# Kernel tuning notes

Measured on AMD Instinct MI355X. Metric: run time of the kernel, lower is better.

Reference implementation:

```python
import jax, jax.numpy as jnp
import numpy as np

L_MAX = 3


def setup_inputs() -> dict:
    key = jax.random.key(0)
    ks = jax.random.split(key, L_MAX + 1)
    n_species, n_samples, n_feat = 2, 1000, 128
    inp = {}
    for l in range(L_MAX + 1):
        inp[f"c_l{l}"] = jax.random.normal(
            ks[l], (n_species, n_samples, 2 * l + 1, n_feat), dtype=jnp.float32
        )
    return inp


def reference(c_l0, c_l1, c_l2, c_l3):
    # For each l: ps = (2l+1)^{-1/2} * sum_m c[..., m, i] * c[..., m, j]
    # i.e. a batched Gram matrix c^T @ c over the m (component) axis,
    # flattened to (S, N, n^2) and concatenated over l.
    parts = []
    for l, c in enumerate((c_l0, c_l1, c_l2, c_l3)):
        cg = (2 * l + 1) ** (-0.5)
        s, n, _, f = c.shape
        ps = cg * jnp.einsum("snmi,snmj->snij", c, c)  # (S, N, f, f)
        parts.append(ps.reshape(s, n, f * f))
    return jnp.concatenate(parts, axis=-1)  # (S, N, (l_max+1)*f^2)
```

## Files before the change

kernel.cpp:

```cpp
#include <hip/hip_runtime.h>


#define NFEAT 128

__device__ __constant__ float kCg[4] = {
    1.0f,
    0.57735026918962576451f,
    0.44721359549995793928f,
    0.37796447300922722721f};

template <int L>
__global__ __launch_bounds__(256) void ps_kernel(const float* __restrict__ c,
                                                 float* __restrict__ out) {
  constexpr int NM = 2 * L + 1;
  __shared__ float sc[NM * NFEAT];

  const int sn  = blockIdx.x;
  const int tid = threadIdx.x;

  const float* src = c + (size_t)sn * (NM * NFEAT);
  if (tid < NM * 32) {
    ((float4*)sc)[tid] = ((const float4*)src)[tid];
  }
  __syncthreads();

  const int j4 = tid & 31;
  const int i0 = tid >> 5;

  float4 b[NM];
#pragma unroll
  for (int m = 0; m < NM; ++m) b[m] = ((const float4*)sc)[m * 32 + j4];

  const float cg = kCg[L];
  float* obase = out + (size_t)sn * (4 * NFEAT * NFEAT) + (size_t)L * (NFEAT * NFEAT);

#pragma unroll
  for (int k = 0; k < 16; ++k) {
    const int i = i0 + 8 * k;
    float4 acc = {0.f, 0.f, 0.f, 0.f};
#pragma unroll
    for (int m = 0; m < NM; ++m) {
      const float a = sc[m * NFEAT + i];
      acc.x += a * b[m].x;
      acc.y += a * b[m].y;
      acc.z += a * b[m].z;
      acc.w += a * b[m].w;
    }
    acc.x *= cg; acc.y *= cg; acc.z *= cg; acc.w *= cg;
    ((float4*)(obase + i * NFEAT))[j4] = acc;
  }
}

extern "C" void kernel_launch(void* const* d_in, const int* in_sizes, int n_in,
                              void* d_out, int out_size, void* d_ws, size_t ws_size,
                              hipStream_t stream) {
  const float* c0 = (const float*)d_in[0];
  const float* c1 = (const float*)d_in[1];
  const float* c2 = (const float*)d_in[2];
  const float* c3 = (const float*)d_in[3];
  float* out = (float*)d_out;

  const int nsn = in_sizes[0] / NFEAT;

  dim3 block(256);
  dim3 grid(nsn);
  ps_kernel<0><<<grid, block, 0, stream>>>(c0, out);
  ps_kernel<1><<<grid, block, 0, stream>>>(c1, out);
  ps_kernel<2><<<grid, block, 0, stream>>>(c2, out);
  ps_kernel<3><<<grid, block, 0, stream>>>(c3, out);
}
```

Before: 507.0 us.

## Fuse per-l launches into one kernel and split rows into chunks

Replaces the four templated per-l launches with a single launch whose grid covers every sample, l value and one of four row chunks. The aim is more blocks in flight and no serialization or tail between launches on a write-bound workload. In exchange, l becomes a runtime value, so the loops are no longer fully unrolled and the b array is dynamically indexed, which may spill to scratch memory.

```diff
diff --git a/kernel.cpp b/kernel.cpp
--- a/kernel.cpp
+++ b/kernel.cpp
@@ -9,17 +9,25 @@
     0.44721359549995793928f,
     0.37796447300922722721f};
 
-template <int L>
-__global__ __launch_bounds__(256) void ps_kernel(const float* __restrict__ c,
-                                                 float* __restrict__ out) {
-  constexpr int NM = 2 * L + 1;
-  __shared__ float sc[NM * NFEAT];
+__global__ __launch_bounds__(256) void ps_fused(const float* __restrict__ c0,
+                                                const float* __restrict__ c1,
+                                                const float* __restrict__ c2,
+                                                const float* __restrict__ c3,
+                                                float* __restrict__ out) {
+  __shared__ float sc[7 * NFEAT];
 
-  const int sn  = blockIdx.x;
-  const int tid = threadIdx.x;
+  const int bid   = blockIdx.x;
+  const int sn    = bid >> 4;
+  const int r     = bid & 15;
+  const int l     = r >> 2;
+  const int chunk = r & 3;
+  const int nm    = 2 * l + 1;
+  const int tid   = threadIdx.x;
 
-  const float* src = c + (size_t)sn * (NM * NFEAT);
-  if (tid < NM * 32) {
+  const float* c = (l == 0) ? c0 : (l == 1) ? c1 : (l == 2) ? c2 : c3;
+
+  const float* src = c + (size_t)sn * ((size_t)nm * NFEAT);
+  if (tid < nm * 32) {
     ((float4*)sc)[tid] = ((const float4*)src)[tid];
   }
   __syncthreads();
@@ -27,20 +35,20 @@
   const int j4 = tid & 31;
   const int i0 = tid >> 5;
 
-  float4 b[NM];
-#pragma unroll
-  for (int m = 0; m < NM; ++m) b[m] = ((const float4*)sc)[m * 32 + j4];
+  float4 b[7];
+  for (int m = 0; m < nm; ++m) b[m] = ((const float4*)sc)[m * 32 + j4];
 
-  const float cg = kCg[L];
-  float* obase = out + (size_t)sn * (4 * NFEAT * NFEAT) + (size_t)L * (NFEAT * NFEAT);
+  const float cg = kCg[l];
+  float* obase = out + (size_t)sn * (4 * NFEAT * NFEAT)
+                     + (size_t)l * (NFEAT * NFEAT)
+                     + (size_t)chunk * 32 * NFEAT;
 
-#pragma unroll
-  for (int k = 0; k < 16; ++k) {
+  for (int k = 0; k < 4; ++k) {
     const int i = i0 + 8 * k;
+    const int row = chunk * 32 + i;
     float4 acc = {0.f, 0.f, 0.f, 0.f};
-#pragma unroll
-    for (int m = 0; m < NM; ++m) {
-      const float a = sc[m * NFEAT + i];
+    for (int m = 0; m < nm; ++m) {
+      const float a = sc[m * NFEAT + row];
       acc.x += a * b[m].x;
       acc.y += a * b[m].y;
       acc.z += a * b[m].z;
@@ -63,9 +71,6 @@
   const int nsn = in_sizes[0] / NFEAT;
 
   dim3 block(256);
-  dim3 grid(nsn);
-  ps_kernel<0><<<grid, block, 0, stream>>>(c0, out);
-  ps_kernel<1><<<grid, block, 0, stream>>>(c1, out);
-  ps_kernel<2><<<grid, block, 0, stream>>>(c2, out);
-  ps_kernel<3><<<grid, block, 0, stream>>>(c3, out);
+  dim3 grid(nsn * 16);
+  ps_fused<<<grid, block, 0, stream>>>(c0, c1, c2, c3, out);
 }
```

Measured after the change: 954.1 us. +88.2%, slower.
